# Optimization experiments

Measured on AMD Instinct MI355X. Metric: run time of the kernel, lower is better.

## Reference

```python
import jax, jax.numpy as jnp
import numpy as np

B, N, C, K, RPE = 8, 4096, 256, 16, 64
LN_EPS = 1e-5


def _layernorm(x, g, b):
    m = jnp.mean(x, axis=-1, keepdims=True)
    v = jnp.mean((x - m) ** 2, axis=-1, keepdims=True)
    return (x - m) * jax.lax.rsqrt(v + LN_EPS) * g + b


def setup_inputs() -> dict:
    key = jax.random.key(0)
    ks = jax.random.split(key, 10)
    def w(k, shape, s=0.02):
        return jax.random.normal(k, shape, jnp.float32) * s
    return {
        "x": jax.random.normal(ks[0], (B, N, C), jnp.float32),
        "pos": jax.random.normal(ks[1], (B, N, 3), jnp.float32),
        "Wq": w(ks[2], (C, C)),
        "Wk": w(ks[3], (C, C)),
        "Wv": w(ks[4], (C, C)),
        "W1": w(ks[5], (3, RPE)), "b1": jnp.zeros((RPE,), jnp.float32),
        "W2": w(ks[6], (RPE, C)), "b2": jnp.zeros((C,), jnp.float32),
        "Wp": w(ks[7], (C, C)), "bp": jnp.zeros((C,), jnp.float32),
        "gq": jnp.ones((C,), jnp.float32), "betaq": jnp.zeros((C,), jnp.float32),
        "gkv": jnp.ones((C,), jnp.float32), "betakv": jnp.zeros((C,), jnp.float32),
    }


def reference(x, pos, Wq, Wk, Wv, W1, b1, W2, b2, Wp, bp, gq, betaq, gkv, betakv):
    scale = C ** (-0.5)
    x_q = _layernorm(x, gq, betaq)
    x_kv = _layernorm(x, gkv, betakv)
    q = x_q @ Wq                      # (B,N,C)
    k = x_kv @ Wk                     # (B,N,C)
    v = x_kv @ Wv                     # (B,N,C)

    # kNN over squared pairwise distances (self has distance 0 on the diagonal)
    a2 = jnp.sum(pos * pos, axis=-1)                       # (B,N)
    dist2 = a2[:, :, None] + a2[:, None, :] - 2.0 * jnp.einsum(
        "bnc,bmc->bnm", pos, pos)                          # (B,N,N)
    dist2 = jnp.maximum(dist2, 0.0)
    eye = jnp.eye(N, dtype=bool)
    dist2 = jnp.where(eye[None], 0.0, dist2)
    _, idx = jax.lax.top_k(-dist2, K)                      # (B,N,K) smallest-k

    gather = jax.vmap(lambda f, i: f[i])                   # (N,C),(N,K)->(N,K,C)
    k_nb = gather(k, idx)                                  # (B,N,K,C)
    v_nb = gather(v, idx)                                  # (B,N,K,C)
    pos_nb = gather(pos, idx)                              # (B,N,K,3)

    rel = pos[:, :, None, :] - pos_nb                      # (B,N,K,3)
    rel_enc = jax.nn.relu(rel @ W1 + b1) @ W2 + b2         # (B,N,K,C)

    attn_logits = jnp.einsum("bnc,bnkc->bnk", q, k_nb) * scale
    attn_logits = attn_logits + jnp.sum(rel_enc, axis=-1) * scale
    attn = jax.nn.softmax(attn_logits, axis=-1)            # (B,N,K)

    out = jnp.einsum("bnk,bnkc->bnc", attn, v_nb)
    out = out @ Wp + bp
    return out
```

## Files before the change

### kernel.cpp

```cpp
#include <hip/hip_runtime.h>
#include <hip/hip_bf16.h>
#include <stdint.h>

#define Bv 8
#define Nv 4096
#define Cv 256
#define Kv 16
#define RPEv 64
#define CAPv 160

typedef short bf16x8 __attribute__((ext_vector_type(8)));
typedef float f32x4 __attribute__((ext_vector_type(4)));

static __device__ __forceinline__ float bf2f(unsigned int u16) {
    union { unsigned int i; float f; } v; v.i = u16 << 16; return v.f;
}
static __device__ __forceinline__ unsigned short f2bf(float f) {
    union { float f; unsigned int i; } v; v.f = f;
    unsigned int x = v.i;
    return (unsigned short)((x + 0x7fffu + ((x >> 16) & 1u)) >> 16);
}
static __device__ __forceinline__ unsigned int umin32(unsigned int a, unsigned int b) { return a < b ? a : b; }
static __device__ __forceinline__ unsigned int umax32(unsigned int a, unsigned int b) { return a > b ? a : b; }
static __device__ __forceinline__ float f16lo(unsigned int u) {
    _Float16 h = __builtin_bit_cast(_Float16, (unsigned short)(u & 0xffffu)); return (float)h;
}
static __device__ __forceinline__ float f16hi(unsigned int u) {
    _Float16 h = __builtin_bit_cast(_Float16, (unsigned short)(u >> 16)); return (float)h;
}
static __device__ __forceinline__ unsigned short f2h(float f) {
    _Float16 h = (_Float16)f; return __builtin_bit_cast(unsigned short, h);
}

__global__ void prep_kernel(const float* __restrict__ W2, const float* __restrict__ b2,
                            float* __restrict__ w2sum, float* __restrict__ b2sum) {
    const int u = threadIdx.x;
    if (u < RPEv) {
        float s = 0.f;
        for (int c = 0; c < Cv; ++c) s += W2[u * Cv + c];
        w2sum[u] = s;
    }
    if (u == 0) {
        float s = 0.f;
        for (int c = 0; c < Cv; ++c) s += b2[c];
        *b2sum = s;
    }
}

__global__ __launch_bounds__(256) void wcast_kernel(
    const float* __restrict__ Wq, const float* __restrict__ Wk,
    const float* __restrict__ Wv, const float* __restrict__ Wp,
    unsigned short* __restrict__ Bt)
{
    const int r = blockIdx.x;
    const int t = threadIdx.x;
    const float* W = (r < 256) ? Wq : (r < 512) ? Wk : (r < 768) ? Wv : Wp;
    const int n = r & 255;
    Bt[r * 256 + t] = f2bf(W[t * 256 + n]);
}

__global__ __launch_bounds__(256) void ln_cast_kernel(
    const float* __restrict__ x,
    const float* __restrict__ gq, const float* __restrict__ bq,
    const float* __restrict__ gkv, const float* __restrict__ bkv,
    unsigned short* __restrict__ Aq, unsigned short* __restrict__ Akv)
{
    const int tid = threadIdx.x;
    const long r0 = (long)blockIdx.x * 8;
    const int row = tid >> 5;
    const int c0 = (tid & 31) * 8;
    const float* xr = x + (r0 + row) * Cv + c0;
    float xv[8];
    *(float4*)&xv[0] = *(const float4*)xr;
    *(float4*)&xv[4] = *(const float4*)(xr + 4);
    float s = 0.f, s2 = 0.f;
#pragma unroll
    for (int i = 0; i < 8; ++i) { s += xv[i]; s2 = fmaf(xv[i], xv[i], s2); }
#pragma unroll
    for (int m = 16; m >= 1; m >>= 1) { s += __shfl_xor(s, m); s2 += __shfl_xor(s2, m); }
    const float mean = s * (1.f / Cv);
    const float var = fmaf(-mean, mean, s2 * (1.f / Cv));
    const float rs = rsqrtf(fmaxf(var, 0.f) + 1e-5f);
    unsigned int pq[4], pk[4];
#pragma unroll
    for (int i = 0; i < 4; ++i) {
        const int c = c0 + 2 * i;
        const float h0 = (xv[2 * i] - mean) * rs;
        const float h1 = (xv[2 * i + 1] - mean) * rs;
        const unsigned int q0 = f2bf(fmaf(h0, gq[c], bq[c]));
        const unsigned int q1 = f2bf(fmaf(h1, gq[c + 1], bq[c + 1]));
        const unsigned int k0 = f2bf(fmaf(h0, gkv[c], bkv[c]));
        const unsigned int k1 = f2bf(fmaf(h1, gkv[c + 1], bkv[c + 1]));
        pq[i] = q0 | (q1 << 16);
        pk[i] = k0 | (k1 << 16);
    }
    const long off = (r0 + row) * Cv + c0;
    *(uint4*)&Aq[off]  = make_uint4(pq[0], pq[1], pq[2], pq[3]);
    *(uint4*)&Akv[off] = make_uint4(pk[0], pk[1], pk[2], pk[3]);
}

__global__ __launch_bounds__(256) void gemm_qkv_kernel(
    const unsigned short* __restrict__ Aq, const unsigned short* __restrict__ Akv,
    const unsigned short* __restrict__ Bt,
    unsigned short* __restrict__ qo, unsigned short* __restrict__ ko,
    unsigned short* __restrict__ vo)
{
    __shared__ unsigned short Albs[2][128 * 64];
    __shared__ unsigned short Blbs[2][128 * 64];

    const int tid = threadIdx.x;
    const int rt = blockIdx.x;
    const int ct = blockIdx.y;
    const unsigned short* A = (ct < 2) ? Aq : Akv;
    const int mat = ct >> 1;
    unsigned short* outp = (mat == 0) ? qo : (mat == 1) ? ko : vo;
    const int colInMat = (ct & 1) * 128;

    const int wid = tid >> 6, l = tid & 63;
    const int wr = wid >> 1, wc = wid & 1;

    int srow[4], scol8[4];
#pragma unroll
    for (int it = 0; it < 4; ++it) {
        const int chunk = it * 256 + tid;
        srow[it] = chunk >> 3;
        scol8[it] = ((chunk & 7) ^ (srow[it] & 7)) * 8;
    }

#define STAGE(buf, ks)                                                                  \
    {                                                                                   \
        _Pragma("unroll")                                                               \
        for (int it = 0; it < 4; ++it) {                                                \
            const unsigned short* ga = A + ((size_t)(rt * 128 + srow[it])) * 256        \
                                         + (ks) * 64 + scol8[it];                       \
            const unsigned short* gb = Bt + ((size_t)(ct * 128 + srow[it])) * 256       \
                                          + (ks) * 64 + scol8[it];                      \
            __builtin_amdgcn_global_load_lds(                                           \
                (const __attribute__((address_space(1))) unsigned int*)(const void*)ga, \
                (__attribute__((address_space(3))) unsigned int*)(void*)                \
                    ((char*)&Albs[buf][0] + (it * 256 + tid) * 16), 16, 0, 0);          \
            __builtin_amdgcn_global_load_lds(                                           \
                (const __attribute__((address_space(1))) unsigned int*)(const void*)gb, \
                (__attribute__((address_space(3))) unsigned int*)(void*)                \
                    ((char*)&Blbs[buf][0] + (it * 256 + tid) * 16), 16, 0, 0);          \
        }                                                                               \
    }

    f32x4 acc[4][4];
#pragma unroll
    for (int m = 0; m < 4; ++m)
#pragma unroll
        for (int n = 0; n < 4; ++n) acc[m][n] = (f32x4){0.f, 0.f, 0.f, 0.f};

    STAGE(0, 0);
    __syncthreads();

    for (int ks = 0; ks < 4; ++ks) {
        const int cur = ks & 1;
        if (ks < 3) STAGE(cur ^ 1, ks + 1);
#pragma unroll
        for (int kk = 0; kk < 2; ++kk) {
            bf16x8 a[4], b[4];
#pragma unroll
            for (int m = 0; m < 4; ++m) {
                const int row = wr * 64 + m * 16 + (l & 15);
                const int byte = row * 128 + ((((kk * 4 + (l >> 4)) * 16)) ^ ((row & 7) << 4));
                a[m] = *(const bf16x8*)((const char*)&Albs[cur][0] + byte);
            }
#pragma unroll
            for (int n = 0; n < 4; ++n) {
                const int row = wc * 64 + n * 16 + (l & 15);
                const int byte = row * 128 + ((((kk * 4 + (l >> 4)) * 16)) ^ ((row & 7) << 4));
                b[n] = *(const bf16x8*)((const char*)&Blbs[cur][0] + byte);
            }
#pragma unroll
            for (int m = 0; m < 4; ++m)
#pragma unroll
                for (int n = 0; n < 4; ++n)
                    acc[m][n] = __builtin_amdgcn_mfma_f32_16x16x32_bf16(a[m], b[n], acc[m][n], 0, 0, 0);
        }
        __syncthreads();
    }

#pragma unroll
    for (int m = 0; m < 4; ++m) {
#pragma unroll
        for (int n = 0; n < 4; ++n) {
#pragma unroll
            for (int j = 0; j < 4; ++j) {
                const int row = rt * 128 + wr * 64 + m * 16 + (l >> 4) * 4 + j;
                const int col = colInMat + wc * 64 + n * 16 + (l & 15);
                outp[(size_t)row * 256 + col] = f2bf(acc[m][n][j]);
            }
        }
    }
#undef STAGE
}

__global__ __launch_bounds__(256) void gemm_proj_kernel(
    const unsigned short* __restrict__ Ab, const unsigned short* __restrict__ Btp,
    const float* __restrict__ bp, float* __restrict__ out)
{
    __shared__ unsigned short Albs[2][128 * 64];
    __shared__ unsigned short Blbs[2][128 * 64];

    const int tid = threadIdx.x;
    const int rt = blockIdx.x;
    const int ct = blockIdx.y;

    const int wid = tid >> 6, l = tid & 63;
    const int wr = wid >> 1, wc = wid & 1;

    int srow[4], scol8[4];
#pragma unroll
    for (int it = 0; it < 4; ++it) {
        const int chunk = it * 256 + tid;
        srow[it] = chunk >> 3;
        scol8[it] = ((chunk & 7) ^ (srow[it] & 7)) * 8;
    }

#define STAGE(buf, ks)                                                                  \
    {                                                                                   \
        _Pragma("unroll")                                                               \
        for (int it = 0; it < 4; ++it) {                                                \
            const unsigned short* ga = Ab + ((size_t)(rt * 128 + srow[it])) * 256       \
                                          + (ks) * 64 + scol8[it];                      \
            const unsigned short* gb = Btp + ((size_t)(ct * 128 + srow[it])) * 256      \
                                           + (ks) * 64 + scol8[it];                     \
            __builtin_amdgcn_global_load_lds(                                           \
                (const __attribute__((address_space(1))) unsigned int*)(const void*)ga, \
                (__attribute__((address_space(3))) unsigned int*)(void*)                \
                    ((char*)&Albs[buf][0] + (it * 256 + tid) * 16), 16, 0, 0);          \
            __builtin_amdgcn_global_load_lds(                                           \
                (const __attribute__((address_space(1))) unsigned int*)(const void*)gb, \
                (__attribute__((address_space(3))) unsigned int*)(void*)                \
                    ((char*)&Blbs[buf][0] + (it * 256 + tid) * 16), 16, 0, 0);          \
        }                                                                               \
    }

    f32x4 acc[4][4];
#pragma unroll
    for (int m = 0; m < 4; ++m)
#pragma unroll
        for (int n = 0; n < 4; ++n) acc[m][n] = (f32x4){0.f, 0.f, 0.f, 0.f};

    STAGE(0, 0);
    __syncthreads();

    for (int ks = 0; ks < 4; ++ks) {
        const int cur = ks & 1;
        if (ks < 3) STAGE(cur ^ 1, ks + 1);
#pragma unroll
        for (int kk = 0; kk < 2; ++kk) {
            bf16x8 a[4], b[4];
#pragma unroll
            for (int m = 0; m < 4; ++m) {
                const int row = wr * 64 + m * 16 + (l & 15);
                const int byte = row * 128 + ((((kk * 4 + (l >> 4)) * 16)) ^ ((row & 7) << 4));
                a[m] = *(const bf16x8*)((const char*)&Albs[cur][0] + byte);
            }
#pragma unroll
            for (int n = 0; n < 4; ++n) {
                const int row = wc * 64 + n * 16 + (l & 15);
                const int byte = row * 128 + ((((kk * 4 + (l >> 4)) * 16)) ^ ((row & 7) << 4));
                b[n] = *(const bf16x8*)((const char*)&Blbs[cur][0] + byte);
            }
#pragma unroll
            for (int m = 0; m < 4; ++m)
#pragma unroll
                for (int n = 0; n < 4; ++n)
                    acc[m][n] = __builtin_amdgcn_mfma_f32_16x16x32_bf16(a[m], b[n], acc[m][n], 0, 0, 0);
        }
        __syncthreads();
    }

#pragma unroll
    for (int n = 0; n < 4; ++n) {
        const int col = ct * 128 + wc * 64 + n * 16 + (l & 15);
        const float bpv = bp[col];
#pragma unroll
        for (int m = 0; m < 4; ++m) {
#pragma unroll
            for (int j = 0; j < 4; ++j) {
                const int row = rt * 128 + wr * 64 + m * 16 + (l >> 4) * 4 + j;
                out[(size_t)row * 256 + col] = acc[m][n][j] + bpv;
            }
        }
    }
#undef STAGE
}

__global__ __launch_bounds__(256) void knn_kernel(
    const float* __restrict__ pos, int* __restrict__ idx_out)
{
    __shared__ unsigned int pxy[Nv];
    __shared__ unsigned short pzs[Nv];
    __shared__ float4 qf[32];
    __shared__ unsigned int akeys[256 * 3];
    __shared__ unsigned int cnt[32];
    __shared__ unsigned short bufs[32 * CAPv];

    const int tid = threadIdx.x;
    const int ql = tid >> 3;
    const int s  = tid & 7;
    const int q  = blockIdx.x * 32 + ql;
    const int b  = q >> 12;
    const int n  = q & (Nv - 1);
    const float* pb = pos + (size_t)b * Nv * 3;

    for (int i = tid; i < Nv; i += 256) {
        const float px = pb[3 * i], py = pb[3 * i + 1], pz = pb[3 * i + 2];
        pxy[i] = (unsigned int)f2h(px) | ((unsigned int)f2h(py) << 16);
        pzs[i] = f2h(pz);
    }
    __syncthreads();

    const unsigned int sxy = pxy[n];
    const float qx = f16lo(sxy), qy = f16hi(sxy);
    const float qz = f16lo((unsigned int)pzs[n]);

    unsigned int c0k = 0xFFFFFFFFu, c1k = 0xFFFFFFFFu, c2k = 0xFFFFFFFFu;
    for (int t = 0; t < 256; ++t) {
        const int j = 16 * t + 2 * s;
        const uint2 xy = *(const uint2*)&pxy[j];
        const unsigned int zz = *(const unsigned int*)&pzs[j];
        const float dx0 = f16lo(xy.x) - qx, dy0 = f16hi(xy.x) - qy, dz0 = f16lo(zz) - qz;
        const float dx1 = f16lo(xy.y) - qx, dy1 = f16hi(xy.y) - qy, dz1 = f16hi(zz) - qz;
        const float d0 = fmaf(dx0, dx0, fmaf(dy0, dy0, dz0 * dz0));
        const float d1 = fmaf(dx1, dx1, fmaf(dy1, dy1, dz1 * dz1));
        const unsigned int k0 = (__float_as_uint(d0) & 0xFFFFF000u) | (unsigned)j;
        const unsigned int k1 = (__float_as_uint(d1) & 0xFFFFF000u) | (unsigned)(j + 1);
        const unsigned int klo = umin32(k0, k1);
        const unsigned int khi = umax32(k0, k1);
        if (klo < c2k) {
            {
                const unsigned int lo = umin32(c0k, klo);
                const unsigned int hi = umax32(c0k, klo);
                c0k = lo;
                const unsigned int lo1 = umin32(c1k, hi);
                const unsigned int hi1 = umax32(c1k, hi);
                c1k = lo1;
                c2k = umin32(c2k, hi1);
            }
            if (khi < c2k) {
                const unsigned int lo = umin32(c0k, khi);
                const unsigned int hi = umax32(c0k, khi);
                c0k = lo;
                const unsigned int lo1 = umin32(c1k, hi);
                const unsigned int hi1 = umax32(c1k, hi);
                c1k = lo1;
                c2k = umin32(c2k, hi1);
            }
        }
    }
    akeys[tid * 3 + 0] = c0k;
    akeys[tid * 3 + 1] = c1k;
    akeys[tid * 3 + 2] = c2k;
    __syncthreads();

    if (tid < 32) {
        unsigned int sel16[16];
#pragma unroll
        for (int i = 0; i < 16; ++i) sel16[i] = 0xFFFFFFFFu;
        for (int s8 = 0; s8 < 8; ++s8) {
#pragma unroll
            for (int i3 = 0; i3 < 3; ++i3) {
                unsigned int cand = akeys[(8 * tid + s8) * 3 + i3];
                if (cand < sel16[15]) {
#pragma unroll
                    for (int i = 0; i < 16; ++i) {
                        const unsigned int lo = umin32(sel16[i], cand);
                        cand = umax32(sel16[i], cand);
                        sel16[i] = lo;
                    }
                }
            }
        }
        const float tau = __uint_as_float(sel16[15] & 0xFFFFF000u) * 1.12f + 1e-20f;
        const int n2 = (blockIdx.x * 32 + tid) & (Nv - 1);
        const unsigned int qp = pxy[n2];
        qf[tid] = make_float4(f16lo(qp), f16hi(qp), f16lo((unsigned int)pzs[n2]), tau);
        cnt[tid] = 0;
    }
    __syncthreads();

    float cx[16], cy[16], cz[16];
#pragma unroll
    for (int k = 0; k < 16; ++k) {
        const unsigned int u = pxy[tid + (k << 8)];
        cx[k] = f16lo(u); cy[k] = f16hi(u);
        cz[k] = f16lo((unsigned int)pzs[tid + (k << 8)]);
    }
    for (int q2 = 0; q2 < 32; ++q2) {
        const float4 Q = qf[q2];
#pragma unroll
        for (int k = 0; k < 16; ++k) {
            const float dx = cx[k] - Q.x, dy = cy[k] - Q.y, dz = cz[k] - Q.z;
            const float d2 = fmaf(dx, dx, fmaf(dy, dy, dz * dz));
            if (d2 < Q.w) {
                const unsigned int slot = atomicAdd(&cnt[q2], 1u);
                if (slot < CAPv) bufs[q2 * CAPv + slot] = (unsigned short)(tid + (k << 8));
            }
        }
    }
    __syncthreads();

    if (tid < 32) {
        const int q2 = blockIdx.x * 32 + tid;
        const int n2 = q2 & (Nv - 1);
        const int b2 = q2 >> 12;
        const float* pb2 = pos + (size_t)b2 * Nv * 3;
        const double qxd = (double)pb2[3 * n2];
        const double qyd = (double)pb2[3 * n2 + 1];
        const double qzd = (double)pb2[3 * n2 + 2];
        const double a2qd = qxd * qxd + qyd * qyd + qzd * qzd;
        int c = (int)cnt[tid]; if (c > CAPv) c = CAPv;
        unsigned long long sel[Kv];
#pragma unroll
        for (int i = 0; i < Kv; ++i) sel[i] = ~0ull;
        for (int t = 0; t < c; ++t) {
            const int j = bufs[tid * CAPv + t];
            const double cxd = (double)pb2[3 * j];
            const double cyd = (double)pb2[3 * j + 1];
            const double czd = (double)pb2[3 * j + 2];
            const double a2cd = cxd * cxd + cyd * cyd + czd * czd;
            const double ddot = qxd * cxd + qyd * cyd + qzd * czd;
            double dv = (a2qd + a2cd) - 2.0 * ddot;
            dv = (dv < 0.0) ? 0.0 : dv;
            if (j == n2) dv = 0.0;
            union { double d; unsigned long long u; } cv; cv.d = dv;
            const unsigned long long key = (cv.u & ~0xFFFULL) | (unsigned long long)j;
            if (key < sel[Kv - 1]) {
                unsigned long long cc = key;
#pragma unroll
                for (int i = 0; i < Kv; ++i) {
                    const unsigned long long lo = (sel[i] < cc) ? sel[i] : cc;
                    const unsigned long long hi = (sel[i] < cc) ? cc : sel[i];
                    sel[i] = lo; cc = hi;
                }
            }
        }
#pragma unroll
        for (int i = 0; i < Kv; ++i)
            idx_out[(long)q2 * Kv + i] = (int)(sel[i] & 0xFFFull);
    }
}

__global__ __launch_bounds__(256) void attn_core_kernel(
    unsigned short* __restrict__ qb, const unsigned short* __restrict__ kb,
    const unsigned short* __restrict__ vb, const int* __restrict__ idx,
    const float* __restrict__ pos, const float* __restrict__ W1,
    const float* __restrict__ b1, const float* __restrict__ w2sum,
    const float* __restrict__ b2sum)
{
    __shared__ float q_lds[8][Cv];
    __shared__ float lg[8][Kv];
    __shared__ float wgt[8][Kv];
    __shared__ int idx_l[8][Kv];
    __shared__ float W1l[3 * RPEv];
    __shared__ float b1l[RPEv], w2s[RPEv];
    __shared__ float posq[24];
    __shared__ float b2s_l;

    const int tid = threadIdx.x;
    const long r0 = (long)blockIdx.x * 8;
    const int bq = (int)(r0 >> 12);

    {
        float* ql = &q_lds[0][0];
        for (int i = tid; i < 8 * Cv; i += 256) ql[i] = bf2f(qb[r0 * Cv + i]);
    }
    if (tid < 128) ((int*)idx_l)[tid] = idx[r0 * Kv + tid];
    if (tid < 3 * RPEv) W1l[tid] = W1[tid];
    if (tid < RPEv) { b1l[tid] = b1[tid]; w2s[tid] = w2sum[tid]; }
    if (tid < 24) posq[tid] = pos[r0 * 3 + tid];
    if (tid == 0) b2s_l = *b2sum;
    __syncthreads();

    const int g = tid >> 4, l = tid & 15;
    for (int r = 0; r < 8; ++r) {
        const int nb = idx_l[r][g];
        const long gi = (long)bq * Nv + nb;
        const unsigned short* kr = kb + gi * Cv + l * 16;
        const float* qq = &q_lds[r][l * 16];
        const uint4 kA = *(const uint4*)kr;
        const uint4 kB = *(const uint4*)(kr + 8);
        float part = 0.f;
        part = fmaf(qq[0],  bf2f(kA.x & 0xffffu), part);
        part = fmaf(qq[1],  bf2f(kA.x >> 16),     part);
        part = fmaf(qq[2],  bf2f(kA.y & 0xffffu), part);
        part = fmaf(qq[3],  bf2f(kA.y >> 16),     part);
        part = fmaf(qq[4],  bf2f(kA.z & 0xffffu), part);
        part = fmaf(qq[5],  bf2f(kA.z >> 16),     part);
        part = fmaf(qq[6],  bf2f(kA.w & 0xffffu), part);
        part = fmaf(qq[7],  bf2f(kA.w >> 16),     part);
        part = fmaf(qq[8],  bf2f(kB.x & 0xffffu), part);
        part = fmaf(qq[9],  bf2f(kB.x >> 16),     part);
        part = fmaf(qq[10], bf2f(kB.y & 0xffffu), part);
        part = fmaf(qq[11], bf2f(kB.y >> 16),     part);
        part = fmaf(qq[12], bf2f(kB.z & 0xffffu), part);
        part = fmaf(qq[13], bf2f(kB.z >> 16),     part);
        part = fmaf(qq[14], bf2f(kB.w & 0xffffu), part);
        part = fmaf(qq[15], bf2f(kB.w >> 16),     part);
        const float rx = posq[r * 3 + 0] - pos[gi * 3 + 0];
        const float ry = posq[r * 3 + 1] - pos[gi * 3 + 1];
        const float rz = posq[r * 3 + 2] - pos[gi * 3 + 2];
#pragma unroll
        for (int u4 = 0; u4 < 4; ++u4) {
            const int u = l * 4 + u4;
            float h = fmaf(rx, W1l[u], fmaf(ry, W1l[RPEv + u], fmaf(rz, W1l[2 * RPEv + u], b1l[u])));
            h = fmaxf(h, 0.f);
            part = fmaf(h, w2s[u], part);
        }
        part += __shfl_xor(part, 8);
        part += __shfl_xor(part, 4);
        part += __shfl_xor(part, 2);
        part += __shfl_xor(part, 1);
        if (l == 0) lg[r][g] = (part + b2s_l) * 0.0625f;
    }
    __syncthreads();
    if (tid < 128) {
        const int rr = tid >> 4, gg = tid & 15;
        const float v = lg[rr][gg];
        float m = v;
        m = fmaxf(m, __shfl_xor(m, 8)); m = fmaxf(m, __shfl_xor(m, 4));
        m = fmaxf(m, __shfl_xor(m, 2)); m = fmaxf(m, __shfl_xor(m, 1));
        const float e = __expf(v - m);
        float ssum = e;
        ssum += __shfl_xor(ssum, 8); ssum += __shfl_xor(ssum, 4);
        ssum += __shfl_xor(ssum, 2); ssum += __shfl_xor(ssum, 1);
        wgt[rr][gg] = e / ssum;
    }
    __syncthreads();
    {
        const int c = tid;
        for (int r = 0; r < 8; ++r) {
            float acc = 0.f;
#pragma unroll
            for (int t = 0; t < Kv; ++t) {
                const long gi = (long)bq * Nv + idx_l[r][t];
                acc = fmaf(wgt[r][t], bf2f((unsigned)vb[gi * Cv + c]), acc);
            }
            qb[(r0 + r) * Cv + c] = f2bf(acc);
        }
    }
}

extern "C" void kernel_launch(void* const* d_in, const int* in_sizes, int n_in,
                              void* d_out, int out_size, void* d_ws, size_t ws_size,
                              hipStream_t stream) {
    (void)in_sizes; (void)n_in; (void)out_size; (void)ws_size;
    const float* x      = (const float*)d_in[0];
    const float* pos    = (const float*)d_in[1];
    const float* Wq     = (const float*)d_in[2];
    const float* Wk     = (const float*)d_in[3];
    const float* Wv     = (const float*)d_in[4];
    const float* W1     = (const float*)d_in[5];
    const float* b1     = (const float*)d_in[6];
    const float* W2     = (const float*)d_in[7];
    const float* b2     = (const float*)d_in[8];
    const float* Wp     = (const float*)d_in[9];
    const float* bp     = (const float*)d_in[10];
    const float* gq     = (const float*)d_in[11];
    const float* betaq  = (const float*)d_in[12];
    const float* gkv    = (const float*)d_in[13];
    const float* betakv = (const float*)d_in[14];
    float* out = (float*)d_out;

    char* ws = (char*)d_ws;
    unsigned short* qb = (unsigned short*)(ws);
    unsigned short* kb = (unsigned short*)(ws + 16777216);
    unsigned short* vb = (unsigned short*)(ws + 33554432);
    int*   idx   = (int*)  (ws + 50331648);
    unsigned short* Bt = (unsigned short*)(ws + 52428800);
    float* w2sum = (float*)(ws + 52953088);
    float* b2sum = (float*)(ws + 52953344);

    unsigned short* Aq  = (unsigned short*)d_out;
    unsigned short* Akv = (unsigned short*)d_out + 8388608;

    hipLaunchKernelGGL(prep_kernel, dim3(1), dim3(64), 0, stream, W2, b2, w2sum, b2sum);
    hipLaunchKernelGGL(wcast_kernel, dim3(1024), dim3(256), 0, stream, Wq, Wk, Wv, Wp, Bt);
    hipLaunchKernelGGL(ln_cast_kernel, dim3(4096), dim3(256), 0, stream,
                       x, gq, betaq, gkv, betakv, Aq, Akv);
    hipLaunchKernelGGL(gemm_qkv_kernel, dim3(256, 6), dim3(256), 0, stream,
                       Aq, Akv, Bt, qb, kb, vb);
    hipLaunchKernelGGL(knn_kernel, dim3(1024), dim3(256), 0, stream, pos, idx);
    hipLaunchKernelGGL(attn_core_kernel, dim3(4096), dim3(256), 0, stream,
                       qb, kb, vb, idx, pos, W1, b1, w2sum, b2sum);
    hipLaunchKernelGGL(gemm_proj_kernel, dim3(256, 2), dim3(256), 0, stream,
                       qb, Bt + 768 * 256, bp, out);
}
```

Before: 238.4 us.

## Use packed fp16 distance math and per-lane min-3 in kNN prefilter

Switches the kNN candidate filtering to packed half2 arithmetic. Positions are stored as pairs of points per word, and each lane keeps a branchless three-smallest list per fp16 lane, with no index-tagged 32-bit keys. The threshold pass likewise tests two points per packed op. This cuts ALU work and branch divergence in the O(N^2) scan. In exchange, fp16 distance precision and overflow could make the threshold less tight, so more candidates may be collected or the buffer capacity may overflow.

```diff
diff --git a/kernel.cpp b/kernel.cpp
--- a/kernel.cpp
+++ b/kernel.cpp
@@ -11,6 +11,8 @@
 
 typedef short bf16x8 __attribute__((ext_vector_type(8)));
 typedef float f32x4 __attribute__((ext_vector_type(4)));
+typedef _Float16 half2v __attribute__((ext_vector_type(2)));
+typedef unsigned short u16x2 __attribute__((ext_vector_type(2)));
 
 static __device__ __forceinline__ float bf2f(unsigned int u16) {
     union { unsigned int i; float f; } v; v.i = u16 << 16; return v.f;
@@ -22,15 +24,14 @@
 }
 static __device__ __forceinline__ unsigned int umin32(unsigned int a, unsigned int b) { return a < b ? a : b; }
 static __device__ __forceinline__ unsigned int umax32(unsigned int a, unsigned int b) { return a > b ? a : b; }
-static __device__ __forceinline__ float f16lo(unsigned int u) {
-    _Float16 h = __builtin_bit_cast(_Float16, (unsigned short)(u & 0xffffu)); return (float)h;
-}
-static __device__ __forceinline__ float f16hi(unsigned int u) {
-    _Float16 h = __builtin_bit_cast(_Float16, (unsigned short)(u >> 16)); return (float)h;
-}
 static __device__ __forceinline__ unsigned short f2h(float f) {
     _Float16 h = (_Float16)f; return __builtin_bit_cast(unsigned short, h);
 }
+static __device__ __forceinline__ float h2f(unsigned int u) {
+    _Float16 h = __builtin_bit_cast(_Float16, (unsigned short)(u & 0xffffu)); return (float)h;
+}
+static __device__ __forceinline__ half2v bch2(unsigned int u) { return __builtin_bit_cast(half2v, u); }
+static __device__ __forceinline__ unsigned int bcu32(u16x2 v) { return __builtin_bit_cast(unsigned int, v); }
 
 __global__ void prep_kernel(const float* __restrict__ W2, const float* __restrict__ b2,
                             float* __restrict__ w2sum, float* __restrict__ b2sum) {
@@ -293,9 +294,9 @@
 __global__ __launch_bounds__(256) void knn_kernel(
     const float* __restrict__ pos, int* __restrict__ idx_out)
 {
-    __shared__ unsigned int pxy[Nv];
-    __shared__ unsigned short pzs[Nv];
-    __shared__ float4 qf[32];
+    __shared__ uint2 pxy2[Nv / 2];
+    __shared__ unsigned int pz2[Nv / 2];
+    __shared__ uint4 qu[32];
     __shared__ unsigned int akeys[256 * 3];
     __shared__ unsigned int cnt[32];
     __shared__ unsigned short bufs[32 * CAPv];
@@ -308,54 +309,50 @@
     const int n  = q & (Nv - 1);
     const float* pb = pos + (size_t)b * Nv * 3;
 
-    for (int i = tid; i < Nv; i += 256) {
-        const float px = pb[3 * i], py = pb[3 * i + 1], pz = pb[3 * i + 2];
-        pxy[i] = (unsigned int)f2h(px) | ((unsigned int)f2h(py) << 16);
-        pzs[i] = f2h(pz);
-    }
-    __syncthreads();
-
-    const unsigned int sxy = pxy[n];
-    const float qx = f16lo(sxy), qy = f16hi(sxy);
-    const float qz = f16lo((unsigned int)pzs[n]);
-
-    unsigned int c0k = 0xFFFFFFFFu, c1k = 0xFFFFFFFFu, c2k = 0xFFFFFFFFu;
+    for (int i = tid; i < Nv / 2; i += 256) {
+        const float* pp = pb + 6 * i;
+        const float2 u0 = *(const float2*)pp;
+        const float2 u1 = *(const float2*)(pp + 2);
+        const float2 u2 = *(const float2*)(pp + 4);
+        const unsigned int x0 = f2h(u0.x), y0 = f2h(u0.y), z0 = f2h(u1.x);
+        const unsigned int x1 = f2h(u1.y), y1 = f2h(u2.x), z1 = f2h(u2.y);
+        pxy2[i] = make_uint2(x0 | (x1 << 16), y0 | (y1 << 16));
+        pz2[i] = z0 | (z1 << 16);
+    }
+    __syncthreads();
+
+    const int pq = n >> 1;
+    const int hq = (n & 1) * 16;
+    const uint2 qxy = pxy2[pq];
+    const unsigned int qzz = pz2[pq];
+    const unsigned int hx = (qxy.x >> hq) & 0xffffu;
+    const unsigned int hy = (qxy.y >> hq) & 0xffffu;
+    const unsigned int hz = (qzz   >> hq) & 0xffffu;
+    const half2v qxp = bch2(hx | (hx << 16));
+    const half2v qyp = bch2(hy | (hy << 16));
+    const half2v qzp = bch2(hz | (hz << 16));
+
+    u16x2 ch0 = {0x7c00, 0x7c00}, ch1 = ch0, ch2 = ch0;
     for (int t = 0; t < 256; ++t) {
-        const int j = 16 * t + 2 * s;
-        const uint2 xy = *(const uint2*)&pxy[j];
-        const unsigned int zz = *(const unsigned int*)&pzs[j];
-        const float dx0 = f16lo(xy.x) - qx, dy0 = f16hi(xy.x) - qy, dz0 = f16lo(zz) - qz;
-        const float dx1 = f16lo(xy.y) - qx, dy1 = f16hi(xy.y) - qy, dz1 = f16hi(zz) - qz;
-        const float d0 = fmaf(dx0, dx0, fmaf(dy0, dy0, dz0 * dz0));
-        const float d1 = fmaf(dx1, dx1, fmaf(dy1, dy1, dz1 * dz1));
-        const unsigned int k0 = (__float_as_uint(d0) & 0xFFFFF000u) | (unsigned)j;
-        const unsigned int k1 = (__float_as_uint(d1) & 0xFFFFF000u) | (unsigned)(j + 1);
-        const unsigned int klo = umin32(k0, k1);
-        const unsigned int khi = umax32(k0, k1);
-        if (klo < c2k) {
-            {
-                const unsigned int lo = umin32(c0k, klo);
-                const unsigned int hi = umax32(c0k, klo);
-                c0k = lo;
-                const unsigned int lo1 = umin32(c1k, hi);
-                const unsigned int hi1 = umax32(c1k, hi);
-                c1k = lo1;
-                c2k = umin32(c2k, hi1);
-            }
-            if (khi < c2k) {
-                const unsigned int lo = umin32(c0k, khi);
-                const unsigned int hi = umax32(c0k, khi);
-                c0k = lo;
-                const unsigned int lo1 = umin32(c1k, hi);
-                const unsigned int hi1 = umax32(c1k, hi);
-                c1k = lo1;
-                c2k = umin32(c2k, hi1);
-            }
-        }
-    }
-    akeys[tid * 3 + 0] = c0k;
-    akeys[tid * 3 + 1] = c1k;
-    akeys[tid * 3 + 2] = c2k;
+        const int p = 8 * t + s;
+        const uint2 xy = pxy2[p];
+        const unsigned int zz = pz2[p];
+        const half2v dx = bch2(xy.x) - qxp;
+        const half2v dy = bch2(xy.y) - qyp;
+        const half2v dz = bch2(zz) - qzp;
+        const half2v d2 = dx * dx + dy * dy + dz * dz;
+        u16x2 k = __builtin_bit_cast(u16x2, d2);
+        const u16x2 mn0 = __builtin_elementwise_min(ch0, k);
+        const u16x2 mx0 = __builtin_elementwise_max(ch0, k);
+        ch0 = mn0;
+        const u16x2 mn1 = __builtin_elementwise_min(ch1, mx0);
+        const u16x2 mx1 = __builtin_elementwise_max(ch1, mx0);
+        ch1 = mn1;
+        ch2 = __builtin_elementwise_min(ch2, mx1);
+    }
+    akeys[tid * 3 + 0] = bcu32(ch0);
+    akeys[tid * 3 + 1] = bcu32(ch1);
+    akeys[tid * 3 + 2] = bcu32(ch2);
     __syncthreads();
 
     if (tid < 32) {
@@ -365,41 +362,64 @@
         for (int s8 = 0; s8 < 8; ++s8) {
 #pragma unroll
             for (int i3 = 0; i3 < 3; ++i3) {
-                unsigned int cand = akeys[(8 * tid + s8) * 3 + i3];
-                if (cand < sel16[15]) {
-#pragma unroll
-                    for (int i = 0; i < 16; ++i) {
-                        const unsigned int lo = umin32(sel16[i], cand);
-                        cand = umax32(sel16[i], cand);
-                        sel16[i] = lo;
+                const unsigned int v = akeys[(8 * tid + s8) * 3 + i3];
+#pragma unroll
+                for (int h = 0; h < 2; ++h) {
+                    unsigned int cand = (h == 0) ? (v & 0xffffu) : (v >> 16);
+                    if (cand < sel16[15]) {
+#pragma unroll
+                        for (int i = 0; i < 16; ++i) {
+                            const unsigned int lo = umin32(sel16[i], cand);
+                            cand = umax32(sel16[i], cand);
+                            sel16[i] = lo;
+                        }
                     }
                 }
             }
         }
-        const float tau = __uint_as_float(sel16[15] & 0xFFFFF000u) * 1.12f + 1e-20f;
+        const float tauf = h2f(sel16[15]) * 1.12f + 1e-9f;
+        const unsigned int taub = f2h(tauf);
         const int n2 = (blockIdx.x * 32 + tid) & (Nv - 1);
-        const unsigned int qp = pxy[n2];
-        qf[tid] = make_float4(f16lo(qp), f16hi(qp), f16lo((unsigned int)pzs[n2]), tau);
+        const int pq2 = n2 >> 1;
+        const int hq2 = (n2 & 1) * 16;
+        const uint2 qxy2 = pxy2[pq2];
+        const unsigned int qzz2 = pz2[pq2];
+        const unsigned int hx2 = (qxy2.x >> hq2) & 0xffffu;
+        const unsigned int hy2 = (qxy2.y >> hq2) & 0xffffu;
+        const unsigned int hz2 = (qzz2   >> hq2) & 0xffffu;
+        qu[tid] = make_uint4(hx2 | (hx2 << 16), hy2 | (hy2 << 16),
+                             hz2 | (hz2 << 16), taub);
         cnt[tid] = 0;
     }
     __syncthreads();
 
-    float cx[16], cy[16], cz[16];
-#pragma unroll
-    for (int k = 0; k < 16; ++k) {
-        const unsigned int u = pxy[tid + (k << 8)];
-        cx[k] = f16lo(u); cy[k] = f16hi(u);
-        cz[k] = f16lo((unsigned int)pzs[tid + (k << 8)]);
+    uint2 cxy[8]; unsigned int czp[8];
+#pragma unroll
+    for (int k = 0; k < 8; ++k) {
+        cxy[k] = pxy2[tid + (k << 8)];
+        czp[k] = pz2[tid + (k << 8)];
     }
     for (int q2 = 0; q2 < 32; ++q2) {
-        const float4 Q = qf[q2];
-#pragma unroll
-        for (int k = 0; k < 16; ++k) {
-            const float dx = cx[k] - Q.x, dy = cy[k] - Q.y, dz = cz[k] - Q.z;
-            const float d2 = fmaf(dx, dx, fmaf(dy, dy, dz * dz));
-            if (d2 < Q.w) {
+        const uint4 Q = qu[q2];
+        const half2v Qx = bch2(Q.x), Qy = bch2(Q.y), Qz = bch2(Q.z);
+        const unsigned int taub = Q.w;
+#pragma unroll
+        for (int k = 0; k < 8; ++k) {
+            const half2v dx = bch2(cxy[k].x) - Qx;
+            const half2v dy = bch2(cxy[k].y) - Qy;
+            const half2v dz = bch2(czp[k]) - Qz;
+            const half2v d2 = dx * dx + dy * dy + dz * dz;
+            const unsigned int bits = __builtin_bit_cast(unsigned int, d2);
+            const unsigned int lo = bits & 0xffffu;
+            const unsigned int hi = bits >> 16;
+            const int p = tid + (k << 8);
+            if (lo < taub) {
                 const unsigned int slot = atomicAdd(&cnt[q2], 1u);
-                if (slot < CAPv) bufs[q2 * CAPv + slot] = (unsigned short)(tid + (k << 8));
+                if (slot < CAPv) bufs[q2 * CAPv + slot] = (unsigned short)(2 * p);
+            }
+            if (hi < taub) {
+                const unsigned int slot = atomicAdd(&cnt[q2], 1u);
+                if (slot < CAPv) bufs[q2 * CAPv + slot] = (unsigned short)(2 * p + 1);
             }
         }
     }
```

Measured after the change: 208.0 us. 12.7% less time.
